# Kernel optimization log

Measured on AMD Instinct MI355X. Metric: run time of the kernel, lower is better.

## Reference

```python
import jax, jax.numpy as jnp
import numpy as np
import math

D_MODEL = 64
H = 8
DK = D_MODEL // H


def setup_inputs() -> dict:
    key = jax.random.key(0)
    ks = jax.random.split(key, 6)
    B, C, T, N = 8, D_MODEL, 12, 307
    x = jax.random.normal(ks[0], (B, C, T, N), dtype=jnp.float32)
    mask = jax.random.randint(ks[1], (B, N, N), 0, 2, dtype=jnp.int32)
    s = 1.0 / math.sqrt(D_MODEL)
    Wq = jax.random.uniform(ks[2], (D_MODEL, D_MODEL), jnp.float32, -s, s)
    bq = jax.random.uniform(ks[3], (D_MODEL,), jnp.float32, -s, s)
    Wk = jax.random.uniform(ks[4], (D_MODEL, D_MODEL), jnp.float32, -s, s)
    bk = jax.random.uniform(ks[5], (D_MODEL,), jnp.float32, -s, s)
    return {"x": x, "mask": mask, "Wq": Wq, "bq": bq, "Wk": Wk, "bk": bk}


def reference(x, mask, Wq, bq, Wk, bk):
    # x: [B, d_model, T, N] -> [B, T, N, d_model]
    B, C, T, N = x.shape
    xp = jnp.transpose(x, (0, 2, 3, 1))
    # torch Linear: y = x W^T + b
    q = jnp.einsum('btnd,ed->btne', xp, Wq) + bq
    k = jnp.einsum('btnd,ed->btne', xp, Wk) + bk
    # split heads: [B, T, N, h, dk]
    q = q.reshape(B, T, N, H, DK)
    k = k.reshape(B, T, N, H, DK)
    # QK^T per head then sum over heads (einsum 'ijkmn->ijmn'), fused:
    # scores: [B, T, N, N]
    scores = jnp.einsum('btnhd,btmhd->btnm', q, k) / math.sqrt(DK)
    # mask.unsqueeze(1) -> [B, 1, N, N]
    scores = jnp.where(mask[:, None] == 0, jnp.float32(-1e9), scores)
    # softmax over last dim; dropout is identity in eval mode
    return jax.nn.softmax(scores, axis=-1)
```

## Files before the change

### kernel.cpp

```cpp
#include <hip/hip_runtime.h>
#include <math.h>

#define PB 8
#define PT 12
#define PN 307
#define NP 320
#define SCALE 0.35355339059327373f

typedef short bf16x8 __attribute__((ext_vector_type(8)));
typedef float f32x4  __attribute__((ext_vector_type(4)));
typedef int   i32x4u __attribute__((ext_vector_type(4), aligned(4)));
typedef float f32x4u __attribute__((ext_vector_type(4), aligned(4)));

__device__ __forceinline__ unsigned short f32_to_bf16(float v) {
    unsigned u = __float_as_uint(v);
    u += 0x7FFFu + ((u >> 16) & 1u);
    return (unsigned short)(u >> 16);
}

__device__ __forceinline__ bf16x8 pack8(float4 lo, float4 hi) {
    bf16x8 r;
    r[0] = (short)f32_to_bf16(lo.x); r[1] = (short)f32_to_bf16(lo.y);
    r[2] = (short)f32_to_bf16(lo.z); r[3] = (short)f32_to_bf16(lo.w);
    r[4] = (short)f32_to_bf16(hi.x); r[5] = (short)f32_to_bf16(hi.y);
    r[6] = (short)f32_to_bf16(hi.z); r[7] = (short)f32_to_bf16(hi.w);
    return r;
}

__global__ __launch_bounds__(128) void qk_proj_kernel(
    const float* __restrict__ x,
    const float* __restrict__ Wq, const float* __restrict__ bq,
    const float* __restrict__ Wk, const float* __restrict__ bk,
    unsigned short* __restrict__ qws, unsigned short* __restrict__ kws)
{
    const int tid  = threadIdx.x;
    const int lane = tid & 63;
    const int wv   = tid >> 6;
    const int chunk = blockIdx.x % 10;
    const int bt    = blockIdx.x / 10;
    const int b = bt / PT, t = bt % PT;
    const int rlo = lane & 15;
    const int kq  = lane >> 4;
    const int n0  = chunk * 32 + wv * 16;

    const int nn = min(n0 + rlo, PN - 1);
    const float* xrow = x + ((size_t)b * 64 * PT + t) * PN + nn;
    bf16x8 a[2];
    #pragma unroll
    for (int ks = 0; ks < 2; ++ks) {
        #pragma unroll
        for (int j = 0; j < 8; ++j) {
            const int c = ks * 32 + kq * 8 + j;
            a[ks][j] = (short)f32_to_bf16(xrow[(size_t)c * PT * PN]);
        }
    }

    f32x4 accq[4] = {}, acck[4] = {};
    #pragma unroll
    for (int et = 0; et < 4; ++et) {
        const float* wq_r = Wq + (size_t)(et * 16 + rlo) * 64 + kq * 8;
        const float* wk_r = Wk + (size_t)(et * 16 + rlo) * 64 + kq * 8;
        #pragma unroll
        for (int ks = 0; ks < 2; ++ks) {
            const bf16x8 bqf = pack8(*(const float4*)(wq_r + ks * 32),
                                     *(const float4*)(wq_r + ks * 32 + 4));
            const bf16x8 bkf = pack8(*(const float4*)(wk_r + ks * 32),
                                     *(const float4*)(wk_r + ks * 32 + 4));
            accq[et] = __builtin_amdgcn_mfma_f32_16x16x32_bf16(a[ks], bqf, accq[et], 0, 0, 0);
            acck[et] = __builtin_amdgcn_mfma_f32_16x16x32_bf16(a[ks], bkf, acck[et], 0, 0, 0);
        }
    }

    #pragma unroll
    for (int et = 0; et < 4; ++et) {
        const int e = et * 16 + rlo;
        const float bqv = bq[e], bkv = bk[e];
        #pragma unroll
        for (int r = 0; r < 4; ++r) {
            const int n = n0 + kq * 4 + r;
            if (n < PN) {
                qws[((size_t)bt * NP + n) * 64 + e] = f32_to_bf16(accq[et][r] + bqv);
                kws[((size_t)bt * NP + n) * 64 + e] = f32_to_bf16(acck[et][r] + bkv);
            }
        }
    }
}

__global__ __launch_bounds__(256) void attn_kernel(
    const unsigned short* __restrict__ qws,
    const unsigned short* __restrict__ kws,
    const int* __restrict__ mask,
    float* __restrict__ out)
{
    const int tid  = threadIdx.x;
    const int lane = tid & 63;
    const int wv   = tid >> 6;
    const int chunk = blockIdx.x % 5;
    const int bt    = blockIdx.x / 5;
    const int b     = bt / PT;
    const int ng  = chunk * 64 + wv * 16;
    const int nl  = lane & 15;
    const int kq  = lane >> 4;
    const int n   = ng + nl;
    const int nn  = (n < PN) ? n : (PN - 1);

    const bf16x8* qp = (const bf16x8*)(qws + ((size_t)bt * NP + n) * 64 + kq * 8);
    const unsigned short* kbase = kws + ((size_t)bt * NP + nl) * 64 + kq * 8;

    f32x4 acc[20] = {};
    #pragma unroll
    for (int ks = 0; ks < 2; ++ks) {
        const bf16x8 bqf = qp[ks * 4];
        const unsigned short* kb = kbase + ks * 32;
        #pragma unroll
        for (int ct = 0; ct < 20; ++ct) {
            const bf16x8 af = *(const bf16x8*)(kb + (size_t)ct * 16 * 64);
            acc[ct] = __builtin_amdgcn_mfma_f32_16x16x32_bf16(af, bqf, acc[ct], 0, 0, 0);
        }
    }

    const int* mrow = mask + ((size_t)b * PN + nn) * PN;
    float mx = -INFINITY;
    #pragma unroll
    for (int ct = 0; ct < 20; ++ct) {
        const int m0 = ct * 16 + kq * 4;
        const i32x4u mv = *(const i32x4u*)(mrow + m0);
        float sv[4];
        sv[0] = mv[0] ? acc[ct][0] * SCALE : -1e9f;
        sv[1] = mv[1] ? acc[ct][1] * SCALE : -1e9f;
        sv[2] = mv[2] ? acc[ct][2] * SCALE : -1e9f;
        sv[3] = mv[3] ? acc[ct][3] * SCALE : -1e9f;
        if (ct == 19) {
            #pragma unroll
            for (int r = 0; r < 4; ++r)
                if (m0 + r >= PN) sv[r] = -INFINITY;
        }
        #pragma unroll
        for (int r = 0; r < 4; ++r) { acc[ct][r] = sv[r]; mx = fmaxf(mx, sv[r]); }
    }
    mx = fmaxf(mx, __shfl_xor(mx, 16));
    mx = fmaxf(mx, __shfl_xor(mx, 32));

    float sum = 0.f;
    #pragma unroll
    for (int ct = 0; ct < 20; ++ct) {
        #pragma unroll
        for (int r = 0; r < 4; ++r) {
            const float p = __expf(acc[ct][r] - mx);
            acc[ct][r] = p;
            sum += p;
        }
    }
    sum += __shfl_xor(sum, 16);
    sum += __shfl_xor(sum, 32);
    const float inv = 1.0f / sum;

    if (n < PN) {
        float* orow = out + ((size_t)bt * PN + n) * PN;
        #pragma unroll
        for (int ct = 0; ct < 19; ++ct) {
            const int m0 = ct * 16 + kq * 4;
            f32x4u o;
            o[0] = acc[ct][0] * inv; o[1] = acc[ct][1] * inv;
            o[2] = acc[ct][2] * inv; o[3] = acc[ct][3] * inv;
            *(f32x4u*)(orow + m0) = o;
        }
        const int m0 = 304 + kq * 4;
        #pragma unroll
        for (int r = 0; r < 4; ++r)
            if (m0 + r < PN) orow[m0 + r] = acc[19][r] * inv;
    }
}

extern "C" void kernel_launch(void* const* d_in, const int* in_sizes, int n_in,
                              void* d_out, int out_size, void* d_ws, size_t ws_size,
                              hipStream_t stream) {
    const float* x  = (const float*)d_in[0];
    const int* mask = (const int*)d_in[1];
    const float* Wq = (const float*)d_in[2];
    const float* bq = (const float*)d_in[3];
    const float* Wk = (const float*)d_in[4];
    const float* bk = (const float*)d_in[5];
    float* out = (float*)d_out;

    unsigned short* qws = (unsigned short*)d_ws;
    unsigned short* kws = qws + (size_t)96 * NP * 64;

    qk_proj_kernel<<<dim3(96 * 10), dim3(128), 0, stream>>>(x, Wq, bq, Wk, bk, qws, kws);
    attn_kernel<<<dim3(96 * 5), dim3(256), 0, stream>>>(qws, kws, mask, out);
}
```

Before: 108.8 us.

## Split softmax rows across warps with shared-memory reductions; widen projection blocks

The attention kernel now gives each block a single 16-row tile and splits the 20 column tiles across 4 waves, five each. Row max and sum are combined across waves through shared memory and two barriers. This cuts per-thread accumulators from 80 floats to 20 and quadruples the grid, which should raise occupancy and parallelism, at the cost of barrier overhead. The projection kernel also doubles its block size, with waves splitting the output feature dimension, so each wave does half the MFMAs.

```diff
diff --git a/kernel.cpp b/kernel.cpp
--- a/kernel.cpp
+++ b/kernel.cpp
@@ -27,7 +27,7 @@
     return r;
 }
 
-__global__ __launch_bounds__(128) void qk_proj_kernel(
+__global__ __launch_bounds__(256) void qk_proj_kernel(
     const float* __restrict__ x,
     const float* __restrict__ Wq, const float* __restrict__ bq,
     const float* __restrict__ Wk, const float* __restrict__ bk,
@@ -36,12 +36,14 @@
     const int tid  = threadIdx.x;
     const int lane = tid & 63;
     const int wv   = tid >> 6;
+    const int wn   = wv & 1;
+    const int we   = wv >> 1;
     const int chunk = blockIdx.x % 10;
     const int bt    = blockIdx.x / 10;
     const int b = bt / PT, t = bt % PT;
     const int rlo = lane & 15;
     const int kq  = lane >> 4;
-    const int n0  = chunk * 32 + wv * 16;
+    const int n0  = chunk * 32 + wn * 16;
 
     const int nn = min(n0 + rlo, PN - 1);
     const float* xrow = x + ((size_t)b * 64 * PT + t) * PN + nn;
@@ -55,32 +57,33 @@
         }
     }
 
-    f32x4 accq[4] = {}, acck[4] = {};
-    #pragma unroll
-    for (int et = 0; et < 4; ++et) {
-        const float* wq_r = Wq + (size_t)(et * 16 + rlo) * 64 + kq * 8;
-        const float* wk_r = Wk + (size_t)(et * 16 + rlo) * 64 + kq * 8;
+    f32x4 accq[2] = {}, acck[2] = {};
+    #pragma unroll
+    for (int eti = 0; eti < 2; ++eti) {
+        const int e_row = we * 32 + eti * 16 + rlo;
+        const float* wq_r = Wq + (size_t)e_row * 64 + kq * 8;
+        const float* wk_r = Wk + (size_t)e_row * 64 + kq * 8;
         #pragma unroll
         for (int ks = 0; ks < 2; ++ks) {
             const bf16x8 bqf = pack8(*(const float4*)(wq_r + ks * 32),
                                      *(const float4*)(wq_r + ks * 32 + 4));
             const bf16x8 bkf = pack8(*(const float4*)(wk_r + ks * 32),
                                      *(const float4*)(wk_r + ks * 32 + 4));
-            accq[et] = __builtin_amdgcn_mfma_f32_16x16x32_bf16(a[ks], bqf, accq[et], 0, 0, 0);
-            acck[et] = __builtin_amdgcn_mfma_f32_16x16x32_bf16(a[ks], bkf, acck[et], 0, 0, 0);
-        }
-    }
-
-    #pragma unroll
-    for (int et = 0; et < 4; ++et) {
-        const int e = et * 16 + rlo;
+            accq[eti] = __builtin_amdgcn_mfma_f32_16x16x32_bf16(a[ks], bqf, accq[eti], 0, 0, 0);
+            acck[eti] = __builtin_amdgcn_mfma_f32_16x16x32_bf16(a[ks], bkf, acck[eti], 0, 0, 0);
+        }
+    }
+
+    #pragma unroll
+    for (int eti = 0; eti < 2; ++eti) {
+        const int e = we * 32 + eti * 16 + rlo;
         const float bqv = bq[e], bkv = bk[e];
         #pragma unroll
         for (int r = 0; r < 4; ++r) {
             const int n = n0 + kq * 4 + r;
             if (n < PN) {
-                qws[((size_t)bt * NP + n) * 64 + e] = f32_to_bf16(accq[et][r] + bqv);
-                kws[((size_t)bt * NP + n) * 64 + e] = f32_to_bf16(acck[et][r] + bkv);
+                qws[((size_t)bt * NP + n) * 64 + e] = f32_to_bf16(accq[eti][r] + bqv);
+                kws[((size_t)bt * NP + n) * 64 + e] = f32_to_bf16(acck[eti][r] + bkv);
             }
         }
     }
@@ -92,83 +95,97 @@
     const int* __restrict__ mask,
     float* __restrict__ out)
 {
+    __shared__ float redmx[4][16];
+    __shared__ float redsm[4][16];
+
     const int tid  = threadIdx.x;
     const int lane = tid & 63;
-    const int wv   = tid >> 6;
-    const int chunk = blockIdx.x % 5;
-    const int bt    = blockIdx.x / 5;
+    const int wm   = tid >> 6;
+    const int ntile = blockIdx.x % 20;
+    const int bt    = blockIdx.x / 20;
     const int b     = bt / PT;
-    const int ng  = chunk * 64 + wv * 16;
+    const int ng  = ntile * 16;
     const int nl  = lane & 15;
     const int kq  = lane >> 4;
     const int n   = ng + nl;
     const int nn  = (n < PN) ? n : (PN - 1);
 
     const bf16x8* qp = (const bf16x8*)(qws + ((size_t)bt * NP + n) * 64 + kq * 8);
+    const bf16x8 bq0 = qp[0], bq1 = qp[4];
     const unsigned short* kbase = kws + ((size_t)bt * NP + nl) * 64 + kq * 8;
 
-    f32x4 acc[20] = {};
-    #pragma unroll
-    for (int ks = 0; ks < 2; ++ks) {
-        const bf16x8 bqf = qp[ks * 4];
-        const unsigned short* kb = kbase + ks * 32;
-        #pragma unroll
-        for (int ct = 0; ct < 20; ++ct) {
-            const bf16x8 af = *(const bf16x8*)(kb + (size_t)ct * 16 * 64);
-            acc[ct] = __builtin_amdgcn_mfma_f32_16x16x32_bf16(af, bqf, acc[ct], 0, 0, 0);
-        }
+    f32x4 acc[5] = {};
+    #pragma unroll
+    for (int i = 0; i < 5; ++i) {
+        const int ct = wm * 5 + i;
+        const unsigned short* kb = kbase + (size_t)ct * 16 * 64;
+        const bf16x8 a0 = *(const bf16x8*)(kb);
+        const bf16x8 a1 = *(const bf16x8*)(kb + 32);
+        acc[i] = __builtin_amdgcn_mfma_f32_16x16x32_bf16(a0, bq0, acc[i], 0, 0, 0);
+        acc[i] = __builtin_amdgcn_mfma_f32_16x16x32_bf16(a1, bq1, acc[i], 0, 0, 0);
     }
 
     const int* mrow = mask + ((size_t)b * PN + nn) * PN;
     float mx = -INFINITY;
     #pragma unroll
-    for (int ct = 0; ct < 20; ++ct) {
+    for (int i = 0; i < 5; ++i) {
+        const int ct = wm * 5 + i;
         const int m0 = ct * 16 + kq * 4;
         const i32x4u mv = *(const i32x4u*)(mrow + m0);
         float sv[4];
-        sv[0] = mv[0] ? acc[ct][0] * SCALE : -1e9f;
-        sv[1] = mv[1] ? acc[ct][1] * SCALE : -1e9f;
-        sv[2] = mv[2] ? acc[ct][2] * SCALE : -1e9f;
-        sv[3] = mv[3] ? acc[ct][3] * SCALE : -1e9f;
+        sv[0] = mv[0] ? acc[i][0] * SCALE : -1e9f;
+        sv[1] = mv[1] ? acc[i][1] * SCALE : -1e9f;
+        sv[2] = mv[2] ? acc[i][2] * SCALE : -1e9f;
+        sv[3] = mv[3] ? acc[i][3] * SCALE : -1e9f;
         if (ct == 19) {
             #pragma unroll
             for (int r = 0; r < 4; ++r)
                 if (m0 + r >= PN) sv[r] = -INFINITY;
         }
         #pragma unroll
-        for (int r = 0; r < 4; ++r) { acc[ct][r] = sv[r]; mx = fmaxf(mx, sv[r]); }
+        for (int r = 0; r < 4; ++r) { acc[i][r] = sv[r]; mx = fmaxf(mx, sv[r]); }
     }
     mx = fmaxf(mx, __shfl_xor(mx, 16));
     mx = fmaxf(mx, __shfl_xor(mx, 32));
+    if (lane < 16) redmx[wm][lane] = mx;
+    __syncthreads();
+    const float gmx = fmaxf(fmaxf(redmx[0][nl], redmx[1][nl]),
+                            fmaxf(redmx[2][nl], redmx[3][nl]));
 
     float sum = 0.f;
     #pragma unroll
-    for (int ct = 0; ct < 20; ++ct) {
+    for (int i = 0; i < 5; ++i) {
         #pragma unroll
         for (int r = 0; r < 4; ++r) {
-            const float p = __expf(acc[ct][r] - mx);
-            acc[ct][r] = p;
+            const float p = __expf(acc[i][r] - gmx);
+            acc[i][r] = p;
             sum += p;
         }
     }
     sum += __shfl_xor(sum, 16);
     sum += __shfl_xor(sum, 32);
-    const float inv = 1.0f / sum;
+    if (lane < 16) redsm[wm][lane] = sum;
+    __syncthreads();
+    const float inv = 1.0f / (redsm[0][nl] + redsm[1][nl] +
+                              redsm[2][nl] + redsm[3][nl]);
 
     if (n < PN) {
         float* orow = out + ((size_t)bt * PN + n) * PN;
         #pragma unroll
-        for (int ct = 0; ct < 19; ++ct) {
+        for (int i = 0; i < 5; ++i) {
+            const int ct = wm * 5 + i;
             const int m0 = ct * 16 + kq * 4;
-            f32x4u o;
-            o[0] = acc[ct][0] * inv; o[1] = acc[ct][1] * inv;
-            o[2] = acc[ct][2] * inv; o[3] = acc[ct][3] * inv;
-            *(f32x4u*)(orow + m0) = o;
-        }
-        const int m0 = 304 + kq * 4;
-        #pragma unroll
-        for (int r = 0; r < 4; ++r)
-            if (m0 + r < PN) orow[m0 + r] = acc[19][r] * inv;
+            if (ct < 19) {
+                f32x4u o;
+                o[0] = acc[i][0] * inv; o[1] = acc[i][1] * inv;
+                o[2] = acc[i][2] * inv; o[3] = acc[i][3] * inv;
+                *(f32x4u*)(orow + m0) = o;
+            } else {
+                #pragma unroll
+                for (int r = 0; r < 4; ++r)
+                    if (m0 + r < PN) orow[m0 + r] = acc[i][r] * inv;
+            }
+        }
     }
 }
 
@@ -186,6 +203,6 @@
     unsigned short* qws = (unsigned short*)d_ws;
     unsigned short* kws = qws + (size_t)96 * NP * 64;
 
-    qk_proj_kernel<<<dim3(96 * 10), dim3(128), 0, stream>>>(x, Wq, bq, Wk, bk, qws, kws);
-    attn_kernel<<<dim3(96 * 5), dim3(256), 0, stream>>>(qws, kws, mask, out);
-}
+    qk_proj_kernel<<<dim3(96 * 10), dim3(256), 0, stream>>>(x, Wq, bq, Wk, bk, qws, kws);
+    attn_kernel<<<dim3(96 * 20), dim3(256), 0, stream>>>(qws, kws, mask, out);
+}
```

Result: no change. 107.7 us (-1.1%).
